# Kernel optimization log

Hardware: AMD Instinct MI355X
Metric: run time of the kernel (lower is better)

The kernel has to match this reference:

```python
import jax, jax.numpy as jnp
import numpy as np

N = 8192
E = 512
EPS = 1e-12  # F.normalize default eps


def setup_inputs() -> dict:
    key = jax.random.key(0)
    ks = jax.random.split(key, 7)
    scale = 1.0 / np.sqrt(E)  # roughly match nn.Linear init scale
    return {
        "x": jax.random.normal(ks[0], (N, E), dtype=jnp.float32),
        "Wq": jax.random.normal(ks[1], (E, E), dtype=jnp.float32) * scale,
        "bq": jax.random.normal(ks[2], (E,), dtype=jnp.float32) * scale,
        "Wk": jax.random.normal(ks[3], (E, E), dtype=jnp.float32) * scale,
        "bk": jax.random.normal(ks[4], (E,), dtype=jnp.float32) * scale,
        "Wv": jax.random.normal(ks[5], (E, E), dtype=jnp.float32) * scale,
        "bv": jax.random.normal(ks[6], (E,), dtype=jnp.float32) * scale,
    }


def reference(x, Wq, bq, Wk, bk, Wv, bv):
    # torch nn.Linear: y = x @ W^T + b
    q = x @ Wq.T + bq  # [N, E]
    k = x @ Wk.T + bk  # [N, E]
    v = x @ Wv.T + bv  # [N, E]
    s = q @ k.T  # [N, N]
    # F.normalize(s): L2-normalize each row (dim=1), norm clamped to eps
    norm = jnp.maximum(jnp.linalg.norm(s, axis=1, keepdims=True), EPS)
    w = s / norm
    # F.softmax default dim for 2-D input is dim=1
    w = jax.nn.softmax(w, axis=1)
    return w @ v  # [N, E]
```

## Files before the change

kernel.cpp:

```cpp
#include <hip/hip_runtime.h>
#include <hip/hip_bf16.h>

typedef unsigned short u16;
typedef unsigned int u32;
typedef short short8 __attribute__((ext_vector_type(8)));
typedef float fvec4 __attribute__((ext_vector_type(4)));

#define NR 8192
#define ED 512
#define PSTR 264

__device__ inline u16 f2bf(float f) {
    union { float f; unsigned u; } c; c.f = f;
    unsigned u = c.u;
    u += 0x7FFFu + ((u >> 16) & 1u);
    return (u16)(u >> 16);
}
__device__ inline float bf2f(u16 h) {
    union { unsigned u; float f; } c; c.u = ((unsigned)h) << 16; return c.f;
}
__device__ inline short8 load_cvt8(const float* p) {
    const fvec4* q = (const fvec4*)p;
    fvec4 a = q[0], b = q[1];
    short8 r;
    r[0] = (short)f2bf(a[0]); r[1] = (short)f2bf(a[1]);
    r[2] = (short)f2bf(a[2]); r[3] = (short)f2bf(a[3]);
    r[4] = (short)f2bf(b[0]); r[5] = (short)f2bf(b[1]);
    r[6] = (short)f2bf(b[2]); r[7] = (short)f2bf(b[3]);
    return r;
}
__device__ inline void gload16(const void* g, void* l) {
    __builtin_amdgcn_global_load_lds(
        (const __attribute__((address_space(1))) u32*)g,
        (__attribute__((address_space(3))) u32*)l, 16, 0, 0);
}

#define SWZ_SCOL(lane) ((((lane) & 7) ^ ((lane) >> 3)) * 8)
#define SWZ_RD(col, row) ((col) ^ (((row) & 7) * 8))

__global__ __launch_bounds__(256) void cvt_kernel(
    const float* __restrict__ x, const float* __restrict__ Wq,
    const float* __restrict__ Wk, const float* __restrict__ Wv,
    u16* __restrict__ xb, u16* __restrict__ wb)
{
    int tid = blockIdx.x * 256 + threadIdx.x;
    const float* src; u16* dst; int off;
    if (tid < 524288)      { src = x;  dst = xb;          off = tid; }
    else if (tid < 557056) { src = Wq; dst = wb;          off = tid - 524288; }
    else if (tid < 589824) { src = Wk; dst = wb + 262144; off = tid - 557056; }
    else                   { src = Wv; dst = wb + 524288; off = tid - 589824; }
    *(short8*)(dst + (size_t)off * 8) = load_cvt8(src + (size_t)off * 8);
}

__global__ __launch_bounds__(256, 3) void qkv_kernel(
    const u16* __restrict__ xb, const u16* __restrict__ wb,
    const float* __restrict__ bq, const float* __restrict__ bk, const float* __restrict__ bv,
    u16* __restrict__ qb, u16* __restrict__ kb, u16* __restrict__ kT, u16* __restrict__ vT)
{
    __shared__ u16 ldsA[128][64];
    __shared__ u16 ldsB[128][64];

    const int lane = threadIdx.x & 63;
    const int w = threadIdx.x >> 6;
    const int ln = lane & 15;
    const int kg = lane >> 4;
    const int wr = w >> 1, wc = w & 1;
    const int z = blockIdx.z;
    const int R0 = blockIdx.y * 128;
    const int C0 = blockIdx.x * 128;
    const int srow = lane >> 3;
    const int scol = SWZ_SCOL(lane);

    const u16* B = wb + (size_t)z * 262144;
    const float* bias = (z == 0) ? bq : (z == 1) ? bk : bv;

    fvec4 acc[4][4];
    #pragma unroll
    for (int m = 0; m < 4; ++m)
        #pragma unroll
        for (int n = 0; n < 4; ++n) acc[m][n] = (fvec4){0.f, 0.f, 0.f, 0.f};

    for (int kt = 0; kt < 8; ++kt) {
        const int k0 = kt * 64;
        __syncthreads();
        #pragma unroll
        for (int i = 0; i < 4; ++i) {
            const int ra = (i * 4 + w) * 8;
            gload16(xb + (size_t)(R0 + ra + srow) * ED + k0 + scol, &ldsA[ra][0]);
            gload16(B  + (size_t)(C0 + ra + srow) * ED + k0 + scol, &ldsB[ra][0]);
        }
        __syncthreads();
        short8 af[2][4], bf8[2][4];
        #pragma unroll
        for (int kk = 0; kk < 2; ++kk) {
            #pragma unroll
            for (int m = 0; m < 4; ++m) {
                const int row = wr * 64 + m * 16 + ln;
                af[kk][m] = *(const short8*)&ldsA[row][SWZ_RD(kk * 32 + kg * 8, row)];
            }
            #pragma unroll
            for (int n = 0; n < 4; ++n) {
                const int row = wc * 64 + n * 16 + ln;
                bf8[kk][n] = *(const short8*)&ldsB[row][SWZ_RD(kk * 32 + kg * 8, row)];
            }
        }
        #pragma unroll
        for (int kk = 0; kk < 2; ++kk)
            #pragma unroll
            for (int m = 0; m < 4; ++m)
                #pragma unroll
                for (int n = 0; n < 4; ++n)
                    acc[m][n] = __builtin_amdgcn_mfma_f32_16x16x32_bf16(af[kk][m], bf8[kk][n], acc[m][n], 0, 0, 0);
    }

    #pragma unroll
    for (int n = 0; n < 4; ++n) {
        const int gcol = C0 + wc * 64 + n * 16 + ln;
        const float bc = bias[gcol];
        #pragma unroll
        for (int m = 0; m < 4; ++m) {
            #pragma unroll
            for (int r = 0; r < 4; ++r) {
                const int grow = R0 + wr * 64 + m * 16 + kg * 4 + r;
                u16 val = f2bf(acc[m][n][r] + bc);
                if (z == 0) {
                    qb[(size_t)grow * ED + gcol] = val;
                } else if (z == 1) {
                    kb[(size_t)grow * ED + gcol] = val;
                    kT[(size_t)gcol * NR + grow] = val;
                } else {
                    vT[(size_t)gcol * NR + grow] = val;
                }
            }
        }
    }
}

__global__ __launch_bounds__(256) void gram_kernel(
    const u16* __restrict__ kT, u16* __restrict__ Gb)
{
    __shared__ float red[4][64][4];
    const int lane = threadIdx.x & 63;
    const int w = threadIdx.x >> 6;
    const int ln = lane & 15;
    const int kg = lane >> 4;
    const int i0 = (blockIdx.x >> 5) * 16, l0 = (blockIdx.x & 31) * 16;

    fvec4 acc[4];
    #pragma unroll
    for (int c = 0; c < 4; ++c) acc[c] = (fvec4){0.f, 0.f, 0.f, 0.f};
    const u16* arow = kT + (size_t)(i0 + ln) * NR + w * 2048 + kg * 8;
    const u16* brow = kT + (size_t)(l0 + ln) * NR + w * 2048 + kg * 8;
    #pragma unroll 8
    for (int t = 0; t < 64; ++t) {
        acc[t & 3] = __builtin_amdgcn_mfma_f32_16x16x32_bf16(
            *(const short8*)(arow + t * 32), *(const short8*)(brow + t * 32), acc[t & 3], 0, 0, 0);
    }
    fvec4 s = acc[0] + acc[1] + acc[2] + acc[3];
    #pragma unroll
    for (int r = 0; r < 4; ++r) red[w][lane][r] = s[r];
    __syncthreads();
    if (w == 0) {
        #pragma unroll
        for (int r = 0; r < 4; ++r) {
            float tot = red[0][lane][r] + red[1][lane][r] + red[2][lane][r] + red[3][lane][r];
            Gb[(size_t)(i0 + kg * 4 + r) * ED + l0 + ln] = f2bf(tot);
        }
    }
}

__global__ __launch_bounds__(256) void rn_kernel(
    const u16* __restrict__ qb, const u16* __restrict__ Gb, float* __restrict__ rn)
{
    __shared__ float red[4][16];
    const int lane = threadIdx.x & 63;
    const int wv = threadIdx.x >> 6;
    const int ln = lane & 15;
    const int kg = lane >> 4;
    const int m0 = blockIdx.x * 16;

    short8 afr[16];
    const u16* qrow = qb + (size_t)(m0 + ln) * ED + kg * 8;
    #pragma unroll
    for (int t = 0; t < 16; ++t) afr[t] = *(const short8*)(qrow + t * 32);

    float ss[4] = {0.f, 0.f, 0.f, 0.f};
    for (int ee = 0; ee < 8; ++ee) {
        const int e = wv * 8 + ee;
        fvec4 a0 = (fvec4){0.f, 0.f, 0.f, 0.f};
        fvec4 a1 = (fvec4){0.f, 0.f, 0.f, 0.f};
        const u16* grow = Gb + (size_t)(e * 16 + ln) * ED + kg * 8;
        #pragma unroll
        for (int t = 0; t < 16; t += 2) {
            a0 = __builtin_amdgcn_mfma_f32_16x16x32_bf16(afr[t],     *(const short8*)(grow + t * 32),       a0, 0, 0, 0);
            a1 = __builtin_amdgcn_mfma_f32_16x16x32_bf16(afr[t + 1], *(const short8*)(grow + (t + 1) * 32), a1, 0, 0, 0);
        }
        fvec4 acc = a0 + a1;
        #pragma unroll
        for (int r = 0; r < 4; ++r)
            ss[r] += acc[r] * bf2f(qb[(size_t)(m0 + kg * 4 + r) * ED + e * 16 + ln]);
    }
    #pragma unroll
    for (int r = 0; r < 4; ++r) {
        float v = ss[r];
        v += __shfl_xor(v, 1); v += __shfl_xor(v, 2);
        v += __shfl_xor(v, 4); v += __shfl_xor(v, 8);
        ss[r] = v;
    }
    if (ln == 0) {
        #pragma unroll
        for (int r = 0; r < 4; ++r) red[wv][kg * 4 + r] = ss[r];
    }
    __syncthreads();
    if (threadIdx.x < 16) {
        const int row = threadIdx.x;
        const float tot = red[0][row] + red[1][row] + red[2][row] + red[3][row];
        rn[m0 + row] = 1.0f / fmaxf(sqrtf(tot), 1e-12f);
    }
}

__global__ __launch_bounds__(256, 3) void sexp_kernel(
    const u16* __restrict__ qb, const u16* __restrict__ kb,
    const float* __restrict__ rn, u16* __restrict__ P, float* __restrict__ dsum)
{
    __shared__ u16 ldsA[128][64];
    __shared__ u16 ldsB[128][64];

    const int lane = threadIdx.x & 63;
    const int w = threadIdx.x >> 6;
    const int ln = lane & 15;
    const int kg = lane >> 4;
    const int wr = w >> 1, wc = w & 1;
    const int R0 = blockIdx.y * 128;
    const int C0 = blockIdx.x * 128;
    const int srow = lane >> 3;
    const int scol = SWZ_SCOL(lane);

    fvec4 acc[4][4];
    #pragma unroll
    for (int m = 0; m < 4; ++m)
        #pragma unroll
        for (int n = 0; n < 4; ++n) acc[m][n] = (fvec4){0.f, 0.f, 0.f, 0.f};

    for (int kt = 0; kt < 8; ++kt) {
        const int k0 = kt * 64;
        __syncthreads();
        #pragma unroll
        for (int i = 0; i < 4; ++i) {
            const int ra = (i * 4 + w) * 8;
            gload16(qb + (size_t)(R0 + ra + srow) * ED + k0 + scol, &ldsA[ra][0]);
            gload16(kb + (size_t)(C0 + ra + srow) * ED + k0 + scol, &ldsB[ra][0]);
        }
        __syncthreads();
        short8 af[2][4], bf8[2][4];
        #pragma unroll
        for (int kk = 0; kk < 2; ++kk) {
            #pragma unroll
            for (int m = 0; m < 4; ++m) {
                const int row = wr * 64 + m * 16 + ln;
                af[kk][m] = *(const short8*)&ldsA[row][SWZ_RD(kk * 32 + kg * 8, row)];
            }
            #pragma unroll
            for (int n = 0; n < 4; ++n) {
                const int row = wc * 64 + n * 16 + ln;
                bf8[kk][n] = *(const short8*)&ldsB[row][SWZ_RD(kk * 32 + kg * 8, row)];
            }
        }
        #pragma unroll
        for (int kk = 0; kk < 2; ++kk)
            #pragma unroll
            for (int m = 0; m < 4; ++m)
                #pragma unroll
                for (int n = 0; n < 4; ++n)
                    acc[m][n] = __builtin_amdgcn_mfma_f32_16x16x32_bf16(af[kk][m], bf8[kk][n], acc[m][n], 0, 0, 0);
    }

    #pragma unroll
    for (int m = 0; m < 4; ++m) {
        float dpart[4] = {0.f, 0.f, 0.f, 0.f};
        #pragma unroll
        for (int r = 0; r < 4; ++r) {
            const int grow = R0 + wr * 64 + m * 16 + kg * 4 + r;
            const float rv = rn[grow];
            #pragma unroll
            for (int n = 0; n < 4; ++n) {
                const int gcol = C0 + wc * 64 + n * 16 + ln;
                u16 pb = f2bf(__expf(acc[m][n][r] * rv));
                P[(size_t)grow * NR + gcol] = pb;
                dpart[r] += bf2f(pb);
            }
        }
        #pragma unroll
        for (int r = 0; r < 4; ++r) {
            float v = dpart[r];
            v += __shfl_xor(v, 1); v += __shfl_xor(v, 2);
            v += __shfl_xor(v, 4); v += __shfl_xor(v, 8);
            if (ln == 0)
                atomicAdd(&dsum[R0 + wr * 64 + m * 16 + kg * 4 + r], v);
        }
    }
}

__global__ __launch_bounds__(256, 4) void pv_kernel(
    const u16* __restrict__ P, const u16* __restrict__ vT, float* __restrict__ part,
    int ksteps)
{
    __shared__ u16 ldsA[128][64];
    __shared__ u16 ldsB[128][64];

    const int lane = threadIdx.x & 63;
    const int w = threadIdx.x >> 6;
    const int ln = lane & 15;
    const int kg = lane >> 4;
    const int wr = w >> 1, wc = w & 1;
    const int id2 = blockIdx.y * gridDim.x + blockIdx.x;
    const int tile = ((id2 & 7) << 5) + (id2 >> 3);
    const int R0 = (tile >> 2) * 128;
    const int C0 = (tile & 3) * 128;
    const int ks = blockIdx.z;
    const int srow = lane >> 3;
    const int scol = SWZ_SCOL(lane);

    float* pp = part + (size_t)ks * NR * ED;

    fvec4 acc[4][4];
    #pragma unroll
    for (int m = 0; m < 4; ++m)
        #pragma unroll
        for (int n = 0; n < 4; ++n) acc[m][n] = (fvec4){0.f, 0.f, 0.f, 0.f};

    for (int kt = 0; kt < ksteps; ++kt) {
        const int k0 = (ks * ksteps + kt) * 64;
        __syncthreads();
        #pragma unroll
        for (int i = 0; i < 4; ++i) {
            const int ra = (i * 4 + w) * 8;
            gload16(P  + (size_t)(R0 + ra + srow) * NR + k0 + scol, &ldsA[ra][0]);
            gload16(vT + (size_t)(C0 + ra + srow) * NR + k0 + scol, &ldsB[ra][0]);
        }
        __syncthreads();
        short8 af[2][4], bf8[2][4];
        #pragma unroll
        for (int kk = 0; kk < 2; ++kk) {
            #pragma unroll
            for (int m = 0; m < 4; ++m) {
                const int row = wr * 64 + m * 16 + ln;
                af[kk][m] = *(const short8*)&ldsA[row][SWZ_RD(kk * 32 + kg * 8, row)];
            }
            #pragma unroll
            for (int n = 0; n < 4; ++n) {
                const int row = wc * 64 + n * 16 + ln;
                bf8[kk][n] = *(const short8*)&ldsB[row][SWZ_RD(kk * 32 + kg * 8, row)];
            }
        }
        #pragma unroll
        for (int kk = 0; kk < 2; ++kk)
            #pragma unroll
            for (int m = 0; m < 4; ++m)
                #pragma unroll
                for (int n = 0; n < 4; ++n)
                    acc[m][n] = __builtin_amdgcn_mfma_f32_16x16x32_bf16(af[kk][m], bf8[kk][n], acc[m][n], 0, 0, 0);
    }

    #pragma unroll
    for (int m = 0; m < 4; ++m) {
        #pragma unroll
        for (int r = 0; r < 4; ++r) {
            const int grow = R0 + wr * 64 + m * 16 + kg * 4 + r;
            #pragma unroll
            for (int n = 0; n < 4; ++n) {
                const int gcol = C0 + wc * 64 + n * 16 + ln;
                pp[(size_t)grow * ED + gcol] = acc[m][n][r];
            }
        }
    }
}

__global__ __launch_bounds__(256) void reduce_kernel(
    const float* __restrict__ part, const float* __restrict__ dsum,
    float* __restrict__ out, int nsplit)
{
    const size_t idx = ((size_t)blockIdx.x * 256 + threadIdx.x) * 4;
    const int row = (int)(idx >> 9);
    const float iv = 1.0f / dsum[row];
    fvec4 s = *(const fvec4*)(part + idx);
    for (int k = 1; k < nsplit; ++k) {
        fvec4 b = *(const fvec4*)(part + (size_t)k * NR * ED + idx);
        #pragma unroll
        for (int i = 0; i < 4; ++i) s[i] += b[i];
    }
    fvec4 o;
    #pragma unroll
    for (int i = 0; i < 4; ++i) o[i] = s[i] * iv;
    *(fvec4*)(out + idx) = o;
}

__global__ __launch_bounds__(512, 2) void attn_kernel(
    const u16* __restrict__ qb, const u16* __restrict__ kb,
    const u16* __restrict__ vT, const float* __restrict__ rn, float* __restrict__ out)
{
    __shared__ u16 p_lds[2 * 16 * PSTR];
    __shared__ float red[2][4][16];

    const int lane = threadIdx.x & 63;
    const int w = threadIdx.x >> 6;
    const int ln = lane & 15;
    const int kg = lane >> 4;
    const int rh = w >> 2;
    const int jg = w & 3;
    const int R0 = blockIdx.x * 32 + rh * 16;

    short8 afr[16];
    const u16* qrow = qb + (size_t)(R0 + ln) * ED + kg * 8;
    #pragma unroll
    for (int t = 0; t < 16; ++t) afr[t] = *(const short8*)(qrow + t * 32);

    float rnv[4];
    #pragma unroll
    for (int r = 0; r < 4; ++r) rnv[r] = rn[R0 + kg * 4 + r];

    fvec4 oacc[8];
    #pragma unroll
    for (int e = 0; e < 8; ++e) oacc[e] = (fvec4){0.f, 0.f, 0.f, 0.f};
    float dsum[4] = {0.f, 0.f, 0.f, 0.f};

    u16* pw = p_lds + rh * 16 * PSTR;

    for (int c = 0; c < 32; ++c) {
        const int j0 = c * 256 + jg * 64;
        fvec4 acc[4];
        #pragma unroll
        for (int jt = 0; jt < 4; ++jt) acc[jt] = (fvec4){0.f, 0.f, 0.f, 0.f};
        const u16* kbase = kb + (size_t)(j0 + ln) * ED + kg * 8;
        #pragma unroll 4
        for (int t = 0; t < 16; ++t) {
            short8 af = afr[t];
            #pragma unroll
            for (int jt = 0; jt < 4; ++jt) {
                short8 bfr = *(const short8*)(kbase + (size_t)jt * 16 * ED + t * 32);
                acc[jt] = __builtin_amdgcn_mfma_f32_16x16x32_bf16(af, bfr, acc[jt], 0, 0, 0);
            }
        }
        #pragma unroll
        for (int jt = 0; jt < 4; ++jt) {
            #pragma unroll
            for (int r = 0; r < 4; ++r) {
                float p = __expf(acc[jt][r] * rnv[r]);
                dsum[r] += p;
                pw[(kg * 4 + r) * PSTR + jg * 64 + jt * 16 + ln] = f2bf(p);
            }
        }
        __syncthreads();
        const u16* vbase = vT + (size_t)(jg * 128 + ln) * NR + c * 256 + kg * 8;
        const u16* prow = pw + ln * PSTR + kg * 8;
        #pragma unroll
        for (int kk = 0; kk < 8; ++kk) {
            short8 afp = *(const short8*)(prow + kk * 32);
            #pragma unroll
            for (int e = 0; e < 8; ++e) {
                short8 bfr = *(const short8*)(vbase + (size_t)e * 16 * NR + kk * 32);
                oacc[e] = __builtin_amdgcn_mfma_f32_16x16x32_bf16(afp, bfr, oacc[e], 0, 0, 0);
            }
        }
        __syncthreads();
    }

    #pragma unroll
    for (int r = 0; r < 4; ++r) {
        float v = dsum[r];
        v += __shfl_xor(v, 1); v += __shfl_xor(v, 2);
        v += __shfl_xor(v, 4); v += __shfl_xor(v, 8);
        dsum[r] = v;
    }
    if (ln == 0) {
        #pragma unroll
        for (int r = 0; r < 4; ++r) red[rh][jg][kg * 4 + r] = dsum[r];
    }
    __syncthreads();
    float inv[4];
    #pragma unroll
    for (int r = 0; r < 4; ++r) {
        const int row = kg * 4 + r;
        inv[r] = 1.0f / (red[rh][0][row] + red[rh][1][row] + red[rh][2][row] + red[rh][3][row]);
    }
    #pragma unroll
    for (int e = 0; e < 8; ++e) {
        #pragma unroll
        for (int r = 0; r < 4; ++r)
            out[(size_t)(R0 + kg * 4 + r) * ED + jg * 128 + e * 16 + ln] = oacc[e][r] * inv[r];
    }
}

extern "C" void kernel_launch(void* const* d_in, const int* in_sizes, int n_in,
                              void* d_out, int out_size, void* d_ws, size_t ws_size,
                              hipStream_t stream) {
    const float* x  = (const float*)d_in[0];
    const float* Wq = (const float*)d_in[1];
    const float* bq = (const float*)d_in[2];
    const float* Wk = (const float*)d_in[3];
    const float* bk = (const float*)d_in[4];
    const float* Wv = (const float*)d_in[5];
    const float* bv = (const float*)d_in[6];
    float* out = (float*)d_out;

    u16* xb = (u16*)d_ws;
    u16* wb = xb + (size_t)NR * ED;
    u16* qb = wb + 3 * 262144;
    u16* kb = qb + (size_t)NR * ED;
    u16* kT = kb + (size_t)NR * ED;
    u16* vT = kT + (size_t)NR * ED;
    u16* Gb = vT + (size_t)NR * ED;
    float* rn   = (float*)(Gb + 262144);
    float* dsum = rn + NR;
    u16* P = (u16*)(dsum + NR);

    const size_t need = (size_t)((u16*)(dsum + NR) - (u16*)d_ws) * 2 + (size_t)NR * NR * 2;
    const size_t need4 = need + (size_t)4 * NR * ED * sizeof(float);

    cvt_kernel<<<2432, 256, 0, stream>>>(x, Wq, Wk, Wv, xb, wb);
    dim3 g1(ED / 128, NR / 128, 3);
    qkv_kernel<<<g1, 256, 0, stream>>>(xb, wb, bq, bk, bv, qb, kb, kT, vT);
    gram_kernel<<<1024, 256, 0, stream>>>(kT, Gb);
    rn_kernel<<<512, 256, 0, stream>>>(qb, Gb, rn);

    if (ws_size >= need) {
        hipMemsetAsync(dsum, 0, NR * sizeof(float), stream);
        dim3 gs(NR / 128, NR / 128);
        sexp_kernel<<<gs, 256, 0, stream>>>(qb, kb, rn, P, dsum);

        int nsplit; float* part;
        if (ws_size >= need4) {
            nsplit = 4;
            part = (float*)(P + (size_t)NR * NR);
        } else {
            nsplit = 2;
            part = (float*)d_ws;
        }
        dim3 gp(ED / 128, NR / 128, nsplit);
        pv_kernel<<<gp, 256, 0, stream>>>(P, vT, part, 128 / nsplit);
        reduce_kernel<<<NR * ED / 4 / 256, 256, 0, stream>>>(part, dsum, out, nsplit);
    } else {
        attn_kernel<<<NR / 32, 512, 0, stream>>>(qb, kb, vT, rn, out);
    }
}
```

Measured before the change: 334.4 us.

## Double-buffer LDS in pv_kernel with K=32 stages to overlap loads and MFMA

```diff
diff --git a/kernel.cpp b/kernel.cpp
--- a/kernel.cpp
+++ b/kernel.cpp
@@ -305,8 +305,8 @@
     const u16* __restrict__ P, const u16* __restrict__ vT, float* __restrict__ part,
     int ksteps)
 {
-    __shared__ u16 ldsA[128][64];
-    __shared__ u16 ldsB[128][64];
+    __shared__ u16 ldsA[2][128][32];
+    __shared__ u16 ldsB[2][128][32];
 
     const int lane = threadIdx.x & 63;
     const int w = threadIdx.x >> 6;
@@ -318,8 +318,8 @@
     const int R0 = (tile >> 2) * 128;
     const int C0 = (tile & 3) * 128;
     const int ks = blockIdx.z;
-    const int srow = lane >> 3;
-    const int scol = SWZ_SCOL(lane);
+    const int srow = lane >> 2;
+    const int scol = (((lane & 3) ^ ((lane >> 3) & 3))) * 8;
 
     float* pp = part + (size_t)ks * NR * ED;
 
@@ -329,37 +329,45 @@
         #pragma unroll
         for (int n = 0; n < 4; ++n) acc[m][n] = (fvec4){0.f, 0.f, 0.f, 0.f};
 
+    const int kbase = ks * ksteps * 32;
+
+    #pragma unroll
+    for (int i = 0; i < 2; ++i) {
+        const int ra = (i * 4 + w) * 16;
+        gload16(P  + (size_t)(R0 + ra + srow) * NR + kbase + scol, &ldsA[0][ra][0]);
+        gload16(vT + (size_t)(C0 + ra + srow) * NR + kbase + scol, &ldsB[0][ra][0]);
+    }
+    __syncthreads();
+
+    int cur = 0;
     for (int kt = 0; kt < ksteps; ++kt) {
-        const int k0 = (ks * ksteps + kt) * 64;
-        __syncthreads();
-        #pragma unroll
-        for (int i = 0; i < 4; ++i) {
-            const int ra = (i * 4 + w) * 8;
-            gload16(P  + (size_t)(R0 + ra + srow) * NR + k0 + scol, &ldsA[ra][0]);
-            gload16(vT + (size_t)(C0 + ra + srow) * NR + k0 + scol, &ldsB[ra][0]);
-        }
-        __syncthreads();
-        short8 af[2][4], bf8[2][4];
-        #pragma unroll
-        for (int kk = 0; kk < 2; ++kk) {
-            #pragma unroll
-            for (int m = 0; m < 4; ++m) {
-                const int row = wr * 64 + m * 16 + ln;
-                af[kk][m] = *(const short8*)&ldsA[row][SWZ_RD(kk * 32 + kg * 8, row)];
-            }
-            #pragma unroll
-            for (int n = 0; n < 4; ++n) {
-                const int row = wc * 64 + n * 16 + ln;
-                bf8[kk][n] = *(const short8*)&ldsB[row][SWZ_RD(kk * 32 + kg * 8, row)];
-            }
-        }
-        #pragma unroll
-        for (int kk = 0; kk < 2; ++kk)
-            #pragma unroll
-            for (int m = 0; m < 4; ++m)
-                #pragma unroll
-                for (int n = 0; n < 4; ++n)
-                    acc[m][n] = __builtin_amdgcn_mfma_f32_16x16x32_bf16(af[kk][m], bf8[kk][n], acc[m][n], 0, 0, 0);
+        if (kt + 1 < ksteps) {
+            const int k0n = kbase + (kt + 1) * 32;
+            #pragma unroll
+            for (int i = 0; i < 2; ++i) {
+                const int ra = (i * 4 + w) * 16;
+                gload16(P  + (size_t)(R0 + ra + srow) * NR + k0n + scol, &ldsA[cur ^ 1][ra][0]);
+                gload16(vT + (size_t)(C0 + ra + srow) * NR + k0n + scol, &ldsB[cur ^ 1][ra][0]);
+            }
+        }
+        short8 af[4], bf8[4];
+        #pragma unroll
+        for (int m = 0; m < 4; ++m) {
+            const int row = wr * 64 + m * 16 + ln;
+            af[m] = *(const short8*)&ldsA[cur][row][(kg ^ ((row >> 1) & 3)) * 8];
+        }
+        #pragma unroll
+        for (int n = 0; n < 4; ++n) {
+            const int row = wc * 64 + n * 16 + ln;
+            bf8[n] = *(const short8*)&ldsB[cur][row][(kg ^ ((row >> 1) & 3)) * 8];
+        }
+        #pragma unroll
+        for (int m = 0; m < 4; ++m)
+            #pragma unroll
+            for (int n = 0; n < 4; ++n)
+                acc[m][n] = __builtin_amdgcn_mfma_f32_16x16x32_bf16(af[m], bf8[n], acc[m][n], 0, 0, 0);
+        __syncthreads();
+        cur ^= 1;
     }
 
     #pragma unroll
@@ -537,7 +545,7 @@
             part = (float*)d_ws;
         }
         dim3 gp(ED / 128, NR / 128, nsplit);
-        pv_kernel<<<gp, 256, 0, stream>>>(P, vT, part, 128 / nsplit);
+        pv_kernel<<<gp, 256, 0, stream>>>(P, vT, part, (NR / nsplit) / 32);
         reduce_kernel<<<NR * ED / 4 / 256, 256, 0, stream>>>(part, dsum, out, nsplit);
     } else {
         attn_kernel<<<NR / 32, 512, 0, stream>>>(qb, kb, vT, rn, out);
```

After: 354.6 us. +6.0%, slower.
